# Optimization experiments

Hardware: AMD Instinct MI355X
Metric: run time of the kernel (lower is better)

Reference implementation:

```python
import jax, jax.numpy as jnp
import numpy as np

N = 100000
E = 1600000
IN, HID, OUT = 2, 32, 1

def setup_inputs() -> dict:
    key = jax.random.key(0)
    ks = jax.random.split(key, 12)
    x = jax.random.normal(ks[0], (N, IN), dtype=jnp.float32)
    edge_index = jax.random.randint(ks[1], (2, E), 0, N, dtype=jnp.int64)
    def lin(k, i, o):
        s = 1.0 / np.sqrt(i)
        return jax.random.uniform(k, (i, o), jnp.float32, -s, s)
    return {
        "x": x,
        "edge_index": edge_index,
        "w1": lin(ks[2], IN, HID), "b1": jnp.zeros((HID,), jnp.float32),
        "g1": jnp.ones((HID,), jnp.float32), "be1": jnp.zeros((HID,), jnp.float32),
        "w2": lin(ks[3], HID, HID), "b2": jnp.zeros((HID,), jnp.float32),
        "g2": jnp.ones((HID,), jnp.float32), "be2": jnp.zeros((HID,), jnp.float32),
        "w3": lin(ks[4], HID, OUT), "b3": jnp.zeros((OUT,), jnp.float32),
    }

def _gcn_conv(x, src, dst, norm, W, b):
    # x: [N, Fin] -> [N, Fout]; symmetric-normalized aggregation incl. self-loops
    h = x @ W                                  # [N, Fout]
    msg = h[src] * norm[:, None]               # gather + scale, [E+N, Fout]
    out = jax.ops.segment_sum(msg, dst, num_segments=N)  # scatter-add
    return out + b

def _layer_norm(x, g, b, eps=1e-5):
    mu = jnp.mean(x, axis=-1, keepdims=True)
    var = jnp.mean(jnp.square(x - mu), axis=-1, keepdims=True)
    return (x - mu) * jax.lax.rsqrt(var + eps) * g + b

def reference(x, edge_index, w1, b1, g1, be1, w2, b2, g2, be2, w3, b3):
    loops = jnp.arange(N, dtype=edge_index.dtype)
    src = jnp.concatenate([edge_index[0], loops])  # [E+N]
    dst = jnp.concatenate([edge_index[1], loops])
    deg = jax.ops.segment_sum(jnp.ones_like(src, dtype=x.dtype), dst, num_segments=N)
    dinv = jnp.where(deg > 0, jax.lax.rsqrt(deg), 0.0)
    norm = dinv[src] * dinv[dst]                   # [E+N]

    h = _gcn_conv(x, src, dst, norm, w1, b1)
    h = jax.nn.relu(_layer_norm(h, g1, be1))       # dropout = identity (eval)
    h = _gcn_conv(h, src, dst, norm, w2, b2)
    h = jax.nn.relu(_layer_norm(h, g2, be2))
    return _gcn_conv(h, src, dst, norm, w3, b3)
```

## Files before the change

### kernel.cpp

```cpp
#include <hip/hip_runtime.h>

constexpr int NN  = 100000;
constexpr int NE  = 1600000;
constexpr int NE4 = NE / 4;
constexpr int HID = 32;
constexpr int NPB = 128;
constexpr int NBIN = (NN + NPB - 1) / NPB;
constexpr int NB  = (NN + 255) / 256;

constexpr int NPART = 8;
constexpr int PPB   = (NBIN + NPART - 1) / NPART;
constexpr int NCHUNK = 120;
constexpr int CAP   = 16;
constexpr int QS    = CAP + 1;


__global__ __launch_bounds__(256) void k_binhist(const int* __restrict__ ei,
                                                 int* __restrict__ bincnt) {
  __shared__ int lh[NBIN];
  int t = threadIdx.x;
  for (int b = t; b < NBIN; b += 256) lh[b] = 0;
  __syncthreads();
  const int4* d4 = (const int4*)(ei + NE);
  for (int q = blockIdx.x * 256 + t; q < NE4; q += gridDim.x * 256) {
    int4 v = d4[q];
    atomicAdd(&lh[v.x >> 7], 1);
    atomicAdd(&lh[v.y >> 7], 1);
    atomicAdd(&lh[v.z >> 7], 1);
    atomicAdd(&lh[v.w >> 7], 1);
  }
  __syncthreads();
  for (int b = t; b < NBIN; b += 256) {
    int v = lh[b];
    if (v) atomicAdd(&bincnt[b], v);
  }
}

__global__ __launch_bounds__(1024) void k_binscan(const int* __restrict__ bincnt,
                                                  int* __restrict__ binptr,
                                                  int* __restrict__ cursor) {
  __shared__ int s[1024];
  int t = threadIdx.x;
  int v = (t < NBIN) ? bincnt[t] : 0;
  s[t] = v;
  __syncthreads();
#pragma unroll
  for (int off = 1; off < 1024; off <<= 1) {
    int add = (t >= off) ? s[t - off] : 0;
    __syncthreads();
    s[t] += add;
    __syncthreads();
  }
  if (t < NBIN) {
    int ex = s[t] - v;
    binptr[t] = ex;
    cursor[t] = ex;
  }
  if (t == NBIN - 1) binptr[NBIN] = s[t];
}

__global__ __launch_bounds__(256) void k_wcscatter(const int* __restrict__ ei,
                                                   int* __restrict__ cursor,
                                                   int* __restrict__ be) {
  __shared__ int q[PPB * QS];
  __shared__ int qn[PPB];
  int t = threadIdx.x;
  int part  = blockIdx.x & (NPART - 1);
  int chunk = blockIdx.x >> 3;
  int b0  = part * PPB;
  int bHi = min(b0 + PPB, NBIN);
  int nb  = bHi - b0;
  for (int b = t; b < nb; b += 256) qn[b] = 0;
  int q0 = (int)((long long)NE4 * chunk / NCHUNK);
  int q1 = (int)((long long)NE4 * (chunk + 1) / NCHUNK);
  const int4* d4 = (const int4*)(ei + NE);
  const int4* s4 = (const int4*)ei;
  __syncthreads();
  for (int qbase = q0; qbase < q1; qbase += 256) {
    int qi = qbase + t;
    int4 dv = make_int4(-1, -1, -1, -1);
    int4 sv = make_int4(0, 0, 0, 0);
    if (qi < q1) { dv = d4[qi]; sv = s4[qi]; }
    int val0 = 0, val1 = 0, val2 = 0, val3 = 0;
    int lb0 = 0, lb1 = 0, lb2 = 0, lb3 = 0;
    unsigned pend = 0;
    {
      int bkt = dv.x >> 7;
      if (dv.x >= 0 && bkt >= b0 && bkt < bHi) {
        val0 = sv.x | ((dv.x & (NPB - 1)) << 17);
        lb0 = bkt - b0;
        int slot = atomicAdd(&qn[lb0], 1);
        if (slot < CAP) q[lb0 * QS + slot] = val0; else pend |= 1u;
      }
    }
    {
      int bkt = dv.y >> 7;
      if (dv.y >= 0 && bkt >= b0 && bkt < bHi) {
        val1 = sv.y | ((dv.y & (NPB - 1)) << 17);
        lb1 = bkt - b0;
        int slot = atomicAdd(&qn[lb1], 1);
        if (slot < CAP) q[lb1 * QS + slot] = val1; else pend |= 2u;
      }
    }
    {
      int bkt = dv.z >> 7;
      if (dv.z >= 0 && bkt >= b0 && bkt < bHi) {
        val2 = sv.z | ((dv.z & (NPB - 1)) << 17);
        lb2 = bkt - b0;
        int slot = atomicAdd(&qn[lb2], 1);
        if (slot < CAP) q[lb2 * QS + slot] = val2; else pend |= 4u;
      }
    }
    {
      int bkt = dv.w >> 7;
      if (dv.w >= 0 && bkt >= b0 && bkt < bHi) {
        val3 = sv.w | ((dv.w & (NPB - 1)) << 17);
        lb3 = bkt - b0;
        int slot = atomicAdd(&qn[lb3], 1);
        if (slot < CAP) q[lb3 * QS + slot] = val3; else pend |= 8u;
      }
    }
    for (;;) {
      __syncthreads();
      for (int b = t; b < nb; b += 256) {
        int n = qn[b];
        if (n >= CAP) {
          int pos = atomicAdd(&cursor[b0 + b], CAP);
#pragma unroll
          for (int j = 0; j < CAP; j++) be[pos + j] = q[b * QS + j];
          qn[b] = 0;
        }
      }
      if (!__syncthreads_or(pend ? 1 : 0)) break;
      if (pend & 1u) {
        int slot = atomicAdd(&qn[lb0], 1);
        if (slot < CAP) { q[lb0 * QS + slot] = val0; pend &= ~1u; }
      }
      if (pend & 2u) {
        int slot = atomicAdd(&qn[lb1], 1);
        if (slot < CAP) { q[lb1 * QS + slot] = val1; pend &= ~2u; }
      }
      if (pend & 4u) {
        int slot = atomicAdd(&qn[lb2], 1);
        if (slot < CAP) { q[lb2 * QS + slot] = val2; pend &= ~4u; }
      }
      if (pend & 8u) {
        int slot = atomicAdd(&qn[lb3], 1);
        if (slot < CAP) { q[lb3 * QS + slot] = val3; pend &= ~8u; }
      }
    }
  }
  for (int b = t; b < nb; b += 256) {
    int n = qn[b];
    if (n > 0) {
      int pos = atomicAdd(&cursor[b0 + b], n);
      for (int j = 0; j < n; j++) be[pos + j] = q[b * QS + j];
    }
  }
}

__global__ __launch_bounds__(256) void k_sort(const int* __restrict__ binptr,
                                              const int* __restrict__ be,
                                              const float* __restrict__ x,
                                              int* __restrict__ csr,
                                              int* __restrict__ rowptr,
                                              int* __restrict__ deg,
                                              float* __restrict__ dinv,
                                              float* __restrict__ xs) {
  __shared__ int hist[NPB];
  __shared__ int excl[NPB];
  __shared__ int cur[NPB];
  int t = threadIdx.x, b = blockIdx.x;
  int e0 = binptr[b], e1 = binptr[b + 1];
  if (t < NPB) hist[t] = 0;
  __syncthreads();
  for (int k = e0 + t; k < e1; k += 256) atomicAdd(&hist[be[k] >> 17], 1);
  __syncthreads();
  if (t < NPB) excl[t] = hist[t];
  __syncthreads();
#pragma unroll
  for (int off = 1; off < NPB; off <<= 1) {
    int add = 0;
    if (t < NPB && t >= off) add = excl[t - off];
    __syncthreads();
    if (t < NPB) excl[t] += add;
    __syncthreads();
  }
  if (t < NPB) {
    int ex = excl[t] - hist[t];
    cur[t] = ex;
    int i = b * NPB + t;
    if (i < NN) {
      int dg = hist[t];
      deg[i] = dg;
      rowptr[i] = e0 + ex;
      float d = rsqrtf((float)dg + 1.0f);
      dinv[i] = d;
      float2 xv = ((const float2*)x)[i];
      ((float2*)xs)[i] = make_float2(d * xv.x, d * xv.y);
    }
  }
  __syncthreads();
  for (int k = e0 + t; k < e1; k += 256) {
    int v = be[k];
    int pos = atomicAdd(&cur[v >> 17], 1);
    csr[e0 + pos] = v & 0x1FFFF;
  }
}


__global__ __launch_bounds__(256) void k_l1(const int* __restrict__ rowptr,
                                            const int* __restrict__ deg,
                                            const int* __restrict__ csr,
                                            const float* __restrict__ dinv,
                                            const float* __restrict__ xs,
                                            const float* __restrict__ w1,
                                            const float* __restrict__ b1,
                                            const float* __restrict__ g1,
                                            const float* __restrict__ be1,
                                            float* __restrict__ h1s) {
  __shared__ float w1s[64], b1s[32], g1s[32], be1s[32];
  int t = threadIdx.x;
  if (t < 64) w1s[t] = w1[t];
  if (t < 32) { b1s[t] = b1[t]; g1s[t] = g1[t]; be1s[t] = be1[t]; }
  __syncthreads();
  int i = blockIdx.x * 256 + t;
  if (i >= NN) return;
  const float2* xs2 = (const float2*)xs;
  float2 sv = xs2[i];
  float in0 = sv.x, in1 = sv.y;
  int r0 = rowptr[i], dg = deg[i];
  int k = 0;
  for (; k + 4 <= dg; k += 4) {
    int s0 = csr[r0 + k], s1 = csr[r0 + k + 1];
    int s2 = csr[r0 + k + 2], s3 = csr[r0 + k + 3];
    float2 v0 = xs2[s0], v1 = xs2[s1], v2 = xs2[s2], v3 = xs2[s3];
    in0 += v0.x; in1 += v0.y;
    in0 += v1.x; in1 += v1.y;
    in0 += v2.x; in1 += v2.y;
    in0 += v3.x; in1 += v3.y;
  }
  for (; k < dg; k++) {
    int s = csr[r0 + k];
    float2 v = xs2[s];
    in0 += v.x; in1 += v.y;
  }
  float di = dinv[i];
  float a0 = di * in0, a1 = di * in1;
  float h[HID];
  float mu = 0.f;
#pragma unroll
  for (int j = 0; j < HID; j++) {
    h[j] = fmaf(a0, w1s[j], fmaf(a1, w1s[32 + j], b1s[j]));
    mu += h[j];
  }
  mu *= (1.0f / HID);
  float var = 0.f;
#pragma unroll
  for (int j = 0; j < HID; j++) { float dd = h[j] - mu; var += dd * dd; }
  var *= (1.0f / HID);
  float rstd = rsqrtf(var + 1e-5f);
  float4* o4 = (float4*)(h1s + (size_t)i * HID);
#pragma unroll
  for (int q = 0; q < 8; q++) {
    float4 v;
    v.x = di * fmaxf(fmaf((h[4 * q]     - mu) * rstd, g1s[4 * q],     be1s[4 * q]),     0.f);
    v.y = di * fmaxf(fmaf((h[4 * q + 1] - mu) * rstd, g1s[4 * q + 1], be1s[4 * q + 1]), 0.f);
    v.z = di * fmaxf(fmaf((h[4 * q + 2] - mu) * rstd, g1s[4 * q + 2], be1s[4 * q + 2]), 0.f);
    v.w = di * fmaxf(fmaf((h[4 * q + 3] - mu) * rstd, g1s[4 * q + 3], be1s[4 * q + 3]), 0.f);
    o4[q] = v;
  }
}

__global__ __launch_bounds__(256) void k_l2(const int* __restrict__ rowptr,
                                            const int* __restrict__ deg,
                                            const int* __restrict__ csr,
                                            const float* __restrict__ dinv,
                                            const float* __restrict__ h1s,
                                            const float* __restrict__ w2,
                                            const float* __restrict__ b2,
                                            const float* __restrict__ g2,
                                            const float* __restrict__ be2,
                                            const float* __restrict__ w3,
                                            float* __restrict__ ps) {
  __shared__ float w2s[HID * HID];
  __shared__ float b2s[32], g2s[32], be2s[32], w3s[32];
  __shared__ float aggl[8][HID];
  int t = threadIdx.x;
  for (int u = t; u < HID * HID; u += 256) w2s[u] = w2[u];
  if (t < 32) { b2s[t] = b2[t]; g2s[t] = g2[t]; be2s[t] = be2[t]; w3s[t] = w3[t]; }
  __syncthreads();
  int g = t >> 5;
  int L = t & 31;
  int i = blockIdx.x * 8 + g;
  int jg = L >> 3, c4 = L & 7;
  const float4* h4 = (const float4*)h1s;
  float ax = 0.f, ay = 0.f, az = 0.f, aw = 0.f;
  if (jg == 0) {
    float4 v = h4[(size_t)i * 8 + c4];
    ax += v.x; ay += v.y; az += v.z; aw += v.w;
  }
  int r0 = rowptr[i], dg = deg[i];
  for (int base = 0; base < dg; base += 16) {
#pragma unroll
    for (int it = 0; it < 4; it++) {
      int kk = base + it * 4 + jg;
      int sv = csr[r0 + kk];
      int s = (kk < dg) ? sv : NN;
      float4 v = h4[(size_t)s * 8 + c4];
      ax += v.x; ay += v.y; az += v.z; aw += v.w;
    }
  }
  ax += __shfl_xor(ax, 8, 32);  ay += __shfl_xor(ay, 8, 32);
  az += __shfl_xor(az, 8, 32);  aw += __shfl_xor(aw, 8, 32);
  ax += __shfl_xor(ax, 16, 32); ay += __shfl_xor(ay, 16, 32);
  az += __shfl_xor(az, 16, 32); aw += __shfl_xor(aw, 16, 32);
  float di = dinv[i];
  if (jg == 0) {
    aggl[g][c4 * 4 + 0] = di * ax;
    aggl[g][c4 * 4 + 1] = di * ay;
    aggl[g][c4 * 4 + 2] = di * az;
    aggl[g][c4 * 4 + 3] = di * aw;
  }
  __syncthreads();
  float h = b2s[L];
#pragma unroll
  for (int k = 0; k < HID; k++) h = fmaf(aggl[g][k], w2s[k * HID + L], h);
  float mu = h;
#pragma unroll
  for (int off = 16; off > 0; off >>= 1) mu += __shfl_xor(mu, off, 32);
  mu *= (1.0f / HID);
  float dd = h - mu;
  float var = dd * dd;
#pragma unroll
  for (int off = 16; off > 0; off >>= 1) var += __shfl_xor(var, off, 32);
  var *= (1.0f / HID);
  float rstd = rsqrtf(var + 1e-5f);
  float v = fmaf(dd * rstd, g2s[L], be2s[L]);
  v = fmaxf(v, 0.0f);
  float pi = v * w3s[L];
#pragma unroll
  for (int off = 16; off > 0; off >>= 1) pi += __shfl_xor(pi, off, 32);
  if (L == 0) ps[i] = di * pi;
}

__global__ __launch_bounds__(256) void k_l3(const int* __restrict__ rowptr,
                                            const int* __restrict__ deg,
                                            const int* __restrict__ csr,
                                            const float* __restrict__ dinv,
                                            const float* __restrict__ ps,
                                            const float* __restrict__ b3,
                                            float* __restrict__ out) {
  int i = blockIdx.x * 256 + threadIdx.x;
  if (i >= NN) return;
  float inner = ps[i];
  int r0 = rowptr[i], dg = deg[i];
  int k = 0;
  for (; k + 4 <= dg; k += 4) {
    float v0 = ps[csr[r0 + k]],     v1 = ps[csr[r0 + k + 1]];
    float v2 = ps[csr[r0 + k + 2]], v3 = ps[csr[r0 + k + 3]];
    inner += v0; inner += v1; inner += v2; inner += v3;
  }
  for (; k < dg; k++) inner += ps[csr[r0 + k]];
  out[i] = fmaf(dinv[i], inner, b3[0]);
}


extern "C" void kernel_launch(void* const* d_in, const int* in_sizes, int n_in,
                              void* d_out, int out_size, void* d_ws, size_t ws_size,
                              hipStream_t stream) {
  const float* x   = (const float*)d_in[0];
  const int*   ei  = (const int*)d_in[1];
  const float* w1  = (const float*)d_in[2];
  const float* b1  = (const float*)d_in[3];
  const float* g1  = (const float*)d_in[4];
  const float* be1 = (const float*)d_in[5];
  const float* w2  = (const float*)d_in[6];
  const float* b2  = (const float*)d_in[7];
  const float* g2  = (const float*)d_in[8];
  const float* be2 = (const float*)d_in[9];
  const float* w3  = (const float*)d_in[10];
  const float* b3  = (const float*)d_in[11];
  float* out = (float*)d_out;

  char* wp = (char*)d_ws;
  auto alloc = [&](size_t bytes) {
    char* r = wp;
    wp += (bytes + 255) & ~size_t(255);
    return r;
  };
  int*   bincnt = (int*)alloc((size_t)NBIN * 4);
  int*   binptr = (int*)alloc((size_t)(NBIN + 1) * 4);
  int*   cursor = (int*)alloc((size_t)NBIN * 4);
  int*   bedge  = (int*)alloc((size_t)NE * 4);
  int*   csr    = (int*)alloc((size_t)(NE + 32) * 4);
  int*   rowptr = (int*)alloc((size_t)NN * 4);
  int*   deg    = (int*)alloc((size_t)NN * 4);
  float* dinv   = (float*)alloc((size_t)NN * 4);
  float* xs     = (float*)alloc((size_t)NN * 2 * 4);
  float* h1s    = (float*)alloc((size_t)(NN + 1) * HID * 4);
  float* ps     = (float*)alloc((size_t)NN * 4);

  hipMemsetAsync(bincnt, 0, (size_t)NBIN * 4, stream);
  hipMemsetAsync(h1s + (size_t)NN * HID, 0, HID * 4, stream);
  k_binhist  <<<NB, 256, 0, stream>>>(ei, bincnt);
  k_binscan  <<<1, 1024, 0, stream>>>(bincnt, binptr, cursor);
  k_wcscatter<<<NCHUNK * NPART, 256, 0, stream>>>(ei, cursor, bedge);
  k_sort     <<<NBIN, 256, 0, stream>>>(binptr, bedge, x, csr, rowptr, deg, dinv, xs);
  k_l1       <<<NB, 256, 0, stream>>>(rowptr, deg, csr, dinv, xs, w1, b1, g1, be1, h1s);
  k_l2       <<<NN / 8, 256, 0, stream>>>(rowptr, deg, csr, dinv, h1s,
                                          w2, b2, g2, be2, w3, ps);
  k_l3       <<<NB, 256, 0, stream>>>(rowptr, deg, csr, dinv, ps, b3, out);
}
```

Measured before the change: 222.7 us.

## Pad CSR rows to 16 and split neighbor gathers across four lanes per node

The CSR build in k_sort now pads each node's adjacency row to a multiple of 16 entries, fills the padding with a dummy index that points at a zeroed row, and offsets each bin by a fixed stride. This lets layer 2 load neighbor indices as aligned int4 vectors with no bounds check. Layers 1 and 3 now give each node four threads that stride through its edges and combine partial sums with shuffles, which adds parallelism and memory-level concurrency for the gathers. The cost is a larger CSR buffer and extra padding writes in the sort kernel.

```diff
diff --git a/kernel.cpp b/kernel.cpp
--- a/kernel.cpp
+++ b/kernel.cpp
@@ -13,6 +13,7 @@
 constexpr int NCHUNK = 120;
 constexpr int CAP   = 16;
 constexpr int QS    = CAP + 1;
+constexpr int BSTRIDE = 2048;
 
 
 __global__ __launch_bounds__(256) void k_binhist(const int* __restrict__ ei,
@@ -170,13 +171,15 @@
   __shared__ int hist[NPB];
   __shared__ int excl[NPB];
   __shared__ int cur[NPB];
+  __shared__ int sbase;
   int t = threadIdx.x, b = blockIdx.x;
   int e0 = binptr[b], e1 = binptr[b + 1];
   if (t < NPB) hist[t] = 0;
+  if (t == 0) sbase = ((binptr[b] + BSTRIDE * b) + 15) & ~15;
   __syncthreads();
   for (int k = e0 + t; k < e1; k += 256) atomicAdd(&hist[be[k] >> 17], 1);
   __syncthreads();
-  if (t < NPB) excl[t] = hist[t];
+  if (t < NPB) excl[t] = (hist[t] + 15) & ~15;
   __syncthreads();
 #pragma unroll
   for (int off = 1; off < NPB; off <<= 1) {
@@ -186,25 +189,28 @@
     if (t < NPB) excl[t] += add;
     __syncthreads();
   }
+  int base = sbase;
   if (t < NPB) {
-    int ex = excl[t] - hist[t];
+    int psz = (hist[t] + 15) & ~15;
+    int ex = excl[t] - psz;
     cur[t] = ex;
     int i = b * NPB + t;
     if (i < NN) {
       int dg = hist[t];
       deg[i] = dg;
-      rowptr[i] = e0 + ex;
+      rowptr[i] = base + ex;
       float d = rsqrtf((float)dg + 1.0f);
       dinv[i] = d;
       float2 xv = ((const float2*)x)[i];
       ((float2*)xs)[i] = make_float2(d * xv.x, d * xv.y);
+      for (int k2 = ex + dg; k2 < ex + psz; k2++) csr[base + k2] = NN;
     }
   }
   __syncthreads();
   for (int k = e0 + t; k < e1; k += 256) {
     int v = be[k];
     int pos = atomicAdd(&cur[v >> 17], 1);
-    csr[e0 + pos] = v & 0x1FFFF;
+    csr[base + pos] = v & 0x1FFFF;
   }
 }
 
@@ -224,51 +230,48 @@
   if (t < 64) w1s[t] = w1[t];
   if (t < 32) { b1s[t] = b1[t]; g1s[t] = g1[t]; be1s[t] = be1[t]; }
   __syncthreads();
-  int i = blockIdx.x * 256 + t;
+  int gid = blockIdx.x * 256 + t;
+  int i = gid >> 2, sub = gid & 3;
   if (i >= NN) return;
   const float2* xs2 = (const float2*)xs;
-  float2 sv = xs2[i];
-  float in0 = sv.x, in1 = sv.y;
+  float in0 = 0.f, in1 = 0.f;
   int r0 = rowptr[i], dg = deg[i];
-  int k = 0;
-  for (; k + 4 <= dg; k += 4) {
-    int s0 = csr[r0 + k], s1 = csr[r0 + k + 1];
-    int s2 = csr[r0 + k + 2], s3 = csr[r0 + k + 3];
-    float2 v0 = xs2[s0], v1 = xs2[s1], v2 = xs2[s2], v3 = xs2[s3];
-    in0 += v0.x; in1 += v0.y;
-    in0 += v1.x; in1 += v1.y;
-    in0 += v2.x; in1 += v2.y;
-    in0 += v3.x; in1 += v3.y;
-  }
-  for (; k < dg; k++) {
+  for (int k = sub; k < dg; k += 4) {
     int s = csr[r0 + k];
     float2 v = xs2[s];
     in0 += v.x; in1 += v.y;
   }
+  in0 += __shfl_xor(in0, 1, 4); in0 += __shfl_xor(in0, 2, 4);
+  in1 += __shfl_xor(in1, 1, 4); in1 += __shfl_xor(in1, 2, 4);
+  float2 sv = xs2[i];
+  in0 += sv.x; in1 += sv.y;
   float di = dinv[i];
   float a0 = di * in0, a1 = di * in1;
-  float h[HID];
+  float h[8];
+  int j0 = sub * 8;
   float mu = 0.f;
 #pragma unroll
-  for (int j = 0; j < HID; j++) {
-    h[j] = fmaf(a0, w1s[j], fmaf(a1, w1s[32 + j], b1s[j]));
+  for (int j = 0; j < 8; j++) {
+    h[j] = fmaf(a0, w1s[j0 + j], fmaf(a1, w1s[32 + j0 + j], b1s[j0 + j]));
     mu += h[j];
   }
+  mu += __shfl_xor(mu, 1, 4); mu += __shfl_xor(mu, 2, 4);
   mu *= (1.0f / HID);
   float var = 0.f;
 #pragma unroll
-  for (int j = 0; j < HID; j++) { float dd = h[j] - mu; var += dd * dd; }
+  for (int j = 0; j < 8; j++) { float dd = h[j] - mu; var += dd * dd; }
+  var += __shfl_xor(var, 1, 4); var += __shfl_xor(var, 2, 4);
   var *= (1.0f / HID);
   float rstd = rsqrtf(var + 1e-5f);
-  float4* o4 = (float4*)(h1s + (size_t)i * HID);
-#pragma unroll
-  for (int q = 0; q < 8; q++) {
+  float4* o4 = (float4*)(h1s + (size_t)i * HID + j0);
+#pragma unroll
+  for (int qq = 0; qq < 2; qq++) {
     float4 v;
-    v.x = di * fmaxf(fmaf((h[4 * q]     - mu) * rstd, g1s[4 * q],     be1s[4 * q]),     0.f);
-    v.y = di * fmaxf(fmaf((h[4 * q + 1] - mu) * rstd, g1s[4 * q + 1], be1s[4 * q + 1]), 0.f);
-    v.z = di * fmaxf(fmaf((h[4 * q + 2] - mu) * rstd, g1s[4 * q + 2], be1s[4 * q + 2]), 0.f);
-    v.w = di * fmaxf(fmaf((h[4 * q + 3] - mu) * rstd, g1s[4 * q + 3], be1s[4 * q + 3]), 0.f);
-    o4[q] = v;
+    v.x = di * fmaxf(fmaf((h[4 * qq]     - mu) * rstd, g1s[j0 + 4 * qq],     be1s[j0 + 4 * qq]),     0.f);
+    v.y = di * fmaxf(fmaf((h[4 * qq + 1] - mu) * rstd, g1s[j0 + 4 * qq + 1], be1s[j0 + 4 * qq + 1]), 0.f);
+    v.z = di * fmaxf(fmaf((h[4 * qq + 2] - mu) * rstd, g1s[j0 + 4 * qq + 2], be1s[j0 + 4 * qq + 2]), 0.f);
+    v.w = di * fmaxf(fmaf((h[4 * qq + 3] - mu) * rstd, g1s[j0 + 4 * qq + 3], be1s[j0 + 4 * qq + 3]), 0.f);
+    o4[qq] = v;
   }
 }
 
@@ -300,16 +303,18 @@
     float4 v = h4[(size_t)i * 8 + c4];
     ax += v.x; ay += v.y; az += v.z; aw += v.w;
   }
-  int r0 = rowptr[i], dg = deg[i];
-  for (int base = 0; base < dg; base += 16) {
-#pragma unroll
-    for (int it = 0; it < 4; it++) {
-      int kk = base + it * 4 + jg;
-      int sv = csr[r0 + kk];
-      int s = (kk < dg) ? sv : NN;
-      float4 v = h4[(size_t)s * 8 + c4];
-      ax += v.x; ay += v.y; az += v.z; aw += v.w;
-    }
+  int r0 = rowptr[i];
+  int dgp = (deg[i] + 15) & ~15;
+  for (int base = 0; base < dgp; base += 16) {
+    int4 iv = *(const int4*)(csr + r0 + base + jg * 4);
+    float4 v0 = h4[(size_t)iv.x * 8 + c4];
+    float4 v1 = h4[(size_t)iv.y * 8 + c4];
+    float4 v2 = h4[(size_t)iv.z * 8 + c4];
+    float4 v3 = h4[(size_t)iv.w * 8 + c4];
+    ax += v0.x; ay += v0.y; az += v0.z; aw += v0.w;
+    ax += v1.x; ay += v1.y; az += v1.z; aw += v1.w;
+    ax += v2.x; ay += v2.y; az += v2.z; aw += v2.w;
+    ax += v3.x; ay += v3.y; az += v3.z; aw += v3.w;
   }
   ax += __shfl_xor(ax, 8, 32);  ay += __shfl_xor(ay, 8, 32);
   az += __shfl_xor(az, 8, 32);  aw += __shfl_xor(aw, 8, 32);
@@ -351,18 +356,16 @@
                                             const float* __restrict__ ps,
                                             const float* __restrict__ b3,
                                             float* __restrict__ out) {
-  int i = blockIdx.x * 256 + threadIdx.x;
+  int gid = blockIdx.x * 256 + threadIdx.x;
+  int i = gid >> 2, sub = gid & 3;
   if (i >= NN) return;
-  float inner = ps[i];
+  float inner = 0.f;
   int r0 = rowptr[i], dg = deg[i];
-  int k = 0;
-  for (; k + 4 <= dg; k += 4) {
-    float v0 = ps[csr[r0 + k]],     v1 = ps[csr[r0 + k + 1]];
-    float v2 = ps[csr[r0 + k + 2]], v3 = ps[csr[r0 + k + 3]];
-    inner += v0; inner += v1; inner += v2; inner += v3;
-  }
-  for (; k < dg; k++) inner += ps[csr[r0 + k]];
-  out[i] = fmaf(dinv[i], inner, b3[0]);
+  for (int k = sub; k < dg; k += 4) inner += ps[csr[r0 + k]];
+  inner += __shfl_xor(inner, 1, 4);
+  inner += __shfl_xor(inner, 2, 4);
+  inner += ps[i];
+  if (sub == 0) out[i] = fmaf(dinv[i], inner, b3[0]);
 }
 
 
@@ -393,7 +396,7 @@
   int*   binptr = (int*)alloc((size_t)(NBIN + 1) * 4);
   int*   cursor = (int*)alloc((size_t)NBIN * 4);
   int*   bedge  = (int*)alloc((size_t)NE * 4);
-  int*   csr    = (int*)alloc((size_t)(NE + 32) * 4);
+  int*   csr    = (int*)alloc((size_t)(NE + (size_t)NBIN * BSTRIDE + 64) * 4);
   int*   rowptr = (int*)alloc((size_t)NN * 4);
   int*   deg    = (int*)alloc((size_t)NN * 4);
   float* dinv   = (float*)alloc((size_t)NN * 4);
@@ -401,14 +404,16 @@
   float* h1s    = (float*)alloc((size_t)(NN + 1) * HID * 4);
   float* ps     = (float*)alloc((size_t)NN * 4);
 
+  int bn4 = (NN * 4 + 255) / 256;
+
   hipMemsetAsync(bincnt, 0, (size_t)NBIN * 4, stream);
   hipMemsetAsync(h1s + (size_t)NN * HID, 0, HID * 4, stream);
   k_binhist  <<<NB, 256, 0, stream>>>(ei, bincnt);
   k_binscan  <<<1, 1024, 0, stream>>>(bincnt, binptr, cursor);
   k_wcscatter<<<NCHUNK * NPART, 256, 0, stream>>>(ei, cursor, bedge);
   k_sort     <<<NBIN, 256, 0, stream>>>(binptr, bedge, x, csr, rowptr, deg, dinv, xs);
-  k_l1       <<<NB, 256, 0, stream>>>(rowptr, deg, csr, dinv, xs, w1, b1, g1, be1, h1s);
+  k_l1       <<<bn4, 256, 0, stream>>>(rowptr, deg, csr, dinv, xs, w1, b1, g1, be1, h1s);
   k_l2       <<<NN / 8, 256, 0, stream>>>(rowptr, deg, csr, dinv, h1s,
                                           w2, b2, g2, be2, w3, ps);
-  k_l3       <<<NB, 256, 0, stream>>>(rowptr, deg, csr, dinv, ps, b3, out);
-}
+  k_l3       <<<bn4, 256, 0, stream>>>(rowptr, deg, csr, dinv, ps, b3, out);
+}
```

Result: no change. 226.6 us (+1.8%).
